# Kernel optimization log

Measured on AMD Instinct MI355X. Metric: run time of the kernel, lower is better.

Reference implementation:

```python
import jax, jax.numpy as jnp
import numpy as np

GX = GY = GZ = 128
VOXEL_DIM = 28  # 1 density + 27 SH coefficients (9 per RGB channel)
NUM_RAYS = 8192
NUM_SAMPLES = 128


def sh_basis(theta, phi):
    """Degree-2 SH basis in the coefficient order used by harmonic():
    [Y_0_0, Y_m1_1, Y_0_1, Y_1_1, Y_m2_2, Y_m1_2, Y_0_2, Y_1_2, Y_2_2]."""
    y00 = 0.5 * jnp.sqrt(1.0 / jnp.pi)
    h3 = 0.5 * jnp.sqrt(3.0 / jnp.pi)
    q5 = 0.25 * jnp.sqrt(5.0 / jnp.pi)
    h15 = 0.5 * jnp.sqrt(15.0 / jnp.pi)
    q15 = 0.25 * jnp.sqrt(15.0 / jnp.pi)
    st, ct = jnp.sin(theta), jnp.cos(theta)
    sp, cp = jnp.sin(phi), jnp.cos(phi)
    return jnp.stack([
        y00 * jnp.ones_like(theta),          # Y_0_0
        h3 * st * sp,                        # Y_m1_1
        h3 * ct,                             # Y_0_1
        h3 * st * cp,                        # Y_1_1
        h15 * st * cp * st * sp,             # Y_m2_2
        h15 * st * sp * ct,                  # Y_m1_2
        q5 * (3.0 * ct * ct - 1.0),          # Y_0_2
        h15 * st * cp * ct,                  # Y_1_2
        q15 * ((st * cp) ** 2 - (st * sp) ** 2),  # Y_2_2
    ])


def trilinear(grid, pos):
    """grid: [GX,GY,GZ,D]; pos: [R,S,3] -> [R,S,D] interpolated features."""
    p0 = jnp.floor(pos).astype(jnp.int32)
    fr = pos - p0.astype(pos.dtype)
    x0, y0, z0 = p0[..., 0], p0[..., 1], p0[..., 2]
    xd, yd, zd = fr[..., 0:1], fr[..., 1:2], fr[..., 2:3]
    c000 = grid[x0, y0, z0]
    c001 = grid[x0, y0, z0 + 1]
    c010 = grid[x0, y0 + 1, z0]
    c011 = grid[x0, y0 + 1, z0 + 1]
    c100 = grid[x0 + 1, y0, z0]
    c101 = grid[x0 + 1, y0, z0 + 1]
    c110 = grid[x0 + 1, y0 + 1, z0]
    c111 = grid[x0 + 1, y0 + 1, z0 + 1]
    c00 = c000 * (1 - xd) + c100 * xd
    c01 = c001 * (1 - xd) + c101 * xd
    c10 = c010 * (1 - xd) + c110 * xd
    c11 = c011 * (1 - xd) + c111 * xd
    c0 = c00 * (1 - yd) + c10 * yd
    c1 = c01 * (1 - yd) + c11 * yd
    return c0 * (1 - zd) + c1 * zd


def setup_inputs() -> dict:
    key = jax.random.key(0)
    k1, k2, k3, k4 = jax.random.split(key, 4)
    voxel_grid = jax.random.uniform(k1, (GX, GY, GZ, VOXEL_DIM), dtype=jnp.float32)
    # sample positions inside [0, G-2] so the +1 corner stays in bounds
    sample_positions = jax.random.uniform(
        k2, (NUM_RAYS, NUM_SAMPLES, 3), dtype=jnp.float32) * (GX - 2)
    sample_distances = jax.random.uniform(
        k3, (NUM_RAYS, NUM_SAMPLES), dtype=jnp.float32) * 0.1
    viewing_angle = jax.random.uniform(k4, (2,), dtype=jnp.float32) * np.pi
    return {
        "voxel_grid": voxel_grid,
        "sample_positions": sample_positions,
        "sample_distances": sample_distances,
        "viewing_angle": viewing_angle,
    }


def reference(voxel_grid, sample_positions, sample_distances, viewing_angle):
    R, S = sample_distances.shape
    feats = trilinear(voxel_grid, sample_positions)          # [R,S,28]
    sigma = feats[..., 0]                                     # [R,S]
    sh_coeffs = feats[..., 1:].reshape(R, S, 3, 9)            # [R,S,3,9]
    basis = sh_basis(viewing_angle[0], viewing_angle[1])      # [9]
    rgb = jnp.einsum('rsck,k->rsc', sh_coeffs, basis)         # [R,S,3]
    tau = sigma * sample_distances                            # [R,S]
    att = jnp.exp(-tau)
    # faithful to channel_opacity_z: transmittance is the CUMULATIVE SUM of
    # exp(-sigma_j * d_j) over j = 0..k (inclusive of current sample)
    transmittance = jnp.cumsum(att, axis=1)
    alpha = 1.0 - att
    weights = transmittance * alpha                           # [R,S]
    return jnp.sum(weights[..., None] * rgb, axis=1)          # [R,3]
```

## Files before the change

kernel.cpp:

```cpp
#include <hip/hip_runtime.h>
#include <math.h>

#define GXD 128
#define GYD 128
#define GZD 128
#define VD 28
#define NRAYS 8192
#define NSAMP 128
#define NVOX (GXD * GYD * GZD)

__global__ __launch_bounds__(256) void predot_grid(
    const float* __restrict__ g,
    const float* __restrict__ ang,
    float4* __restrict__ o)
{
    __shared__ float sb[9];
    if (threadIdx.x == 0) {
        float st, ct, sp, cp;
        sincosf(ang[0], &st, &ct);
        sincosf(ang[1], &sp, &cp);
        sb[0] = 0.28209479177387814f;
        sb[1] = 0.4886025119029199f * st * sp;
        sb[2] = 0.4886025119029199f * ct;
        sb[3] = 0.4886025119029199f * st * cp;
        sb[4] = 1.0925484305920792f * st * cp * st * sp;
        sb[5] = 1.0925484305920792f * st * sp * ct;
        sb[6] = 0.31539156525252005f * (3.0f * ct * ct - 1.0f);
        sb[7] = 1.0925484305920792f * st * cp * ct;
        sb[8] = 0.5462742152960396f * ((st * cp) * (st * cp) - (st * sp) * (st * sp));
    }
    __syncthreads();

    const int v = blockIdx.x * 256 + threadIdx.x;
    const float4* __restrict__ p = (const float4*)(g + (size_t)v * VD);
    float f[28];
    #pragma unroll
    for (int i = 0; i < 7; ++i)
        ((float4*)f)[i] = p[i];

    float r = 0.0f, gg = 0.0f, b = 0.0f;
    #pragma unroll
    for (int k = 0; k < 9; ++k) {
        r  += sb[k] * f[1 + k];
        gg += sb[k] * f[10 + k];
        b  += sb[k] * f[19 + k];
    }
    o[v] = make_float4(f[0], r, gg, b);
}

#define LERP4(a, b, t) make_float4( \
    fmaf((t), (b).x - (a).x, (a).x), \
    fmaf((t), (b).y - (a).y, (a).y), \
    fmaf((t), (b).z - (a).z, (a).z), \
    fmaf((t), (b).w - (a).w, (a).w))

__global__ __launch_bounds__(256) void render(
    const float4* __restrict__ vg,
    const float* __restrict__ pos,
    const float* __restrict__ dist,
    float* __restrict__ out)
{
    __shared__ float4 srgb[2][NSAMP];

    const int tid  = threadIdx.x;
    const int rloc = tid >> 7;
    const int s    = tid & 127;
    const int ray  = blockIdx.x * 2 + rloc;
    const int sidx = ray * NSAMP + s;

    const float px = pos[sidx * 3 + 0];
    const float py = pos[sidx * 3 + 1];
    const float pz = pos[sidx * 3 + 2];
    const int ix = (int)floorf(px);
    const int iy = (int)floorf(py);
    const int iz = (int)floorf(pz);
    const float fx = px - (float)ix;
    const float fy = py - (float)iy;
    const float fz = pz - (float)iz;

    const float4* __restrict__ c = vg + (((size_t)ix * GYD + iy) * GZD + iz);
    const float4 c000 = c[0];
    const float4 c001 = c[1];
    const float4 c010 = c[GZD];
    const float4 c011 = c[GZD + 1];
    const float4 c100 = c[(size_t)GYD * GZD];
    const float4 c101 = c[(size_t)GYD * GZD + 1];
    const float4 c110 = c[(size_t)GYD * GZD + GZD];
    const float4 c111 = c[(size_t)GYD * GZD + GZD + 1];

    const float4 a00 = LERP4(c000, c001, fz);
    const float4 a01 = LERP4(c010, c011, fz);
    const float4 a10 = LERP4(c100, c101, fz);
    const float4 a11 = LERP4(c110, c111, fz);
    const float4 a0  = LERP4(a00, a01, fy);
    const float4 a1  = LERP4(a10, a11, fy);
    const float4 a   = LERP4(a0, a1, fx);

    const float d   = dist[sidx];
    const float att = expf(-a.x * d);
    srgb[rloc][s] = make_float4(att, a.y, a.z, a.w);
    __syncthreads();

    if ((tid & 127) < 64) {
        const int lane = tid & 63;
        const float4 a0v = srgb[rloc][lane];
        const float4 a1v = srgb[rloc][lane + 64];
        const float att0 = a0v.x;
        const float att1 = a1v.x;

        float scan_lo = att0;
        #pragma unroll
        for (int off = 1; off < 64; off <<= 1) {
            const float v = __shfl_up(scan_lo, off, 64);
            if (lane >= off) scan_lo += v;
        }
        const float total_lo = __shfl(scan_lo, 63, 64);

        float scan_hi = att1;
        #pragma unroll
        for (int off = 1; off < 64; off <<= 1) {
            const float v = __shfl_up(scan_hi, off, 64);
            if (lane >= off) scan_hi += v;
        }
        const float w_lo = scan_lo * (1.0f - att0);
        const float w_hi = (total_lo + scan_hi) * (1.0f - att1);

        float o0 = w_lo * a0v.y + w_hi * a1v.y;
        float o1 = w_lo * a0v.z + w_hi * a1v.z;
        float o2 = w_lo * a0v.w + w_hi * a1v.w;

        #pragma unroll
        for (int off = 32; off > 0; off >>= 1) {
            o0 += __shfl_xor(o0, off, 64);
            o1 += __shfl_xor(o1, off, 64);
            o2 += __shfl_xor(o2, off, 64);
        }
        if (lane == 0) {
            out[ray * 3 + 0] = o0;
            out[ray * 3 + 1] = o1;
            out[ray * 3 + 2] = o2;
        }
    }
}

__global__ __launch_bounds__(1024) void plenoxel_fused32(
    const float* __restrict__ grid,
    const float* __restrict__ pos,
    const float* __restrict__ dist,
    const float* __restrict__ ang,
    float* __restrict__ out)
{
    __shared__ float4 srgb[NSAMP];
    const int ray  = blockIdx.x;
    const int tid  = threadIdx.x;
    const int s    = tid >> 3;
    const int subl = tid & 7;
    const int dx   = (subl >> 2) & 1;
    const int dy   = (subl >> 1) & 1;
    const int zh   = subl & 1;

    const float theta = ang[0], phi = ang[1];
    float st, ct, sp, cp;
    sincosf(theta, &st, &ct);
    sincosf(phi,   &sp, &cp);
    float basis[9];
    basis[0] = 0.28209479177387814f;
    basis[1] = 0.4886025119029199f * st * sp;
    basis[2] = 0.4886025119029199f * ct;
    basis[3] = 0.4886025119029199f * st * cp;
    basis[4] = 1.0925484305920792f * st * cp * st * sp;
    basis[5] = 1.0925484305920792f * st * sp * ct;
    basis[6] = 0.31539156525252005f * (3.0f * ct * ct - 1.0f);
    basis[7] = 1.0925484305920792f * st * cp * ct;
    basis[8] = 0.5462742152960396f * ((st * cp) * (st * cp) - (st * sp) * (st * sp));

    const int sidx = ray * NSAMP + s;
    const float px = pos[sidx * 3 + 0];
    const float py = pos[sidx * 3 + 1];
    const float pz = pos[sidx * 3 + 2];
    const int ix = (int)floorf(px);
    const int iy = (int)floorf(py);
    const int iz = (int)floorf(pz);
    const float fx = px - (float)ix;
    const float fy = py - (float)iy;
    const float fz = pz - (float)iz;

    const float w = (dx ? fx : 1.0f - fx) *
                    (dy ? fy : 1.0f - fy) *
                    (zh ? fz : 1.0f - fz);

    const int base = (((ix + dx) * GYD + (iy + dy)) * GZD + (iz + zh)) * VD;
    const float4* __restrict__ q = (const float4*)(grid + base);
    float f[28];
    #pragma unroll
    for (int i = 0; i < 7; ++i)
        ((float4*)f)[i] = q[i];

    float psig = w * f[0];
    float pr = 0.0f, pg = 0.0f, pb = 0.0f;
    #pragma unroll
    for (int k = 0; k < 9; ++k) {
        pr += basis[k] * f[1 + k];
        pg += basis[k] * f[10 + k];
        pb += basis[k] * f[19 + k];
    }
    pr *= w; pg *= w; pb *= w;

    #pragma unroll
    for (int off = 1; off < 8; off <<= 1) {
        psig += __shfl_xor(psig, off, 64);
        pr   += __shfl_xor(pr,   off, 64);
        pg   += __shfl_xor(pg,   off, 64);
        pb   += __shfl_xor(pb,   off, 64);
    }
    if (subl == 0) srgb[s] = make_float4(psig, pr, pg, pb);
    __syncthreads();

    if (tid < 64) {
        const int lane = tid;
        const float4 a0 = srgb[lane];
        const float4 a1 = srgb[lane + 64];
        const float d0 = dist[ray * NSAMP + lane];
        const float d1 = dist[ray * NSAMP + lane + 64];
        const float att0 = expf(-a0.x * d0);
        const float att1 = expf(-a1.x * d1);

        float scan_lo = att0;
        #pragma unroll
        for (int off = 1; off < 64; off <<= 1) {
            const float v = __shfl_up(scan_lo, off, 64);
            if (lane >= off) scan_lo += v;
        }
        const float total_lo = __shfl(scan_lo, 63, 64);
        float scan_hi = att1;
        #pragma unroll
        for (int off = 1; off < 64; off <<= 1) {
            const float v = __shfl_up(scan_hi, off, 64);
            if (lane >= off) scan_hi += v;
        }
        const float w_lo = scan_lo * (1.0f - att0);
        const float w_hi = (total_lo + scan_hi) * (1.0f - att1);

        float o0 = w_lo * a0.y + w_hi * a1.y;
        float o1 = w_lo * a0.z + w_hi * a1.z;
        float o2 = w_lo * a0.w + w_hi * a1.w;
        #pragma unroll
        for (int off = 32; off > 0; off >>= 1) {
            o0 += __shfl_xor(o0, off, 64);
            o1 += __shfl_xor(o1, off, 64);
            o2 += __shfl_xor(o2, off, 64);
        }
        if (lane == 0) {
            out[ray * 3 + 0] = o0;
            out[ray * 3 + 1] = o1;
            out[ray * 3 + 2] = o2;
        }
    }
}

extern "C" void kernel_launch(void* const* d_in, const int* in_sizes, int n_in,
                              void* d_out, int out_size, void* d_ws, size_t ws_size,
                              hipStream_t stream) {
    const float* grid = (const float*)d_in[0];
    const float* pos  = (const float*)d_in[1];
    const float* dist = (const float*)d_in[2];
    const float* ang  = (const float*)d_in[3];
    float* out = (float*)d_out;

    const size_t need = (size_t)NVOX * sizeof(float4);
    if (ws_size >= need) {
        float4* vg = (float4*)d_ws;
        predot_grid<<<NVOX / 256, 256, 0, stream>>>(grid, ang, vg);
        render<<<NRAYS / 2, 256, 0, stream>>>(vg, pos, dist, out);
    } else {
        plenoxel_fused32<<<NRAYS, 1024, 0, stream>>>(grid, pos, dist, ang, out);
    }
}
```

Baseline: 399.8 us.

## Store pre-dotted grid as fp16 in 2x2 xy-interleaved layout

The precomputed per-voxel (sigma, r, g, b) grid is now stored as four half values (8 bytes) instead of float4. It also uses a layout that interleaves 2x2 xy columns along z, so all eight trilinear corners fall in nearby cache lines. This halves workspace traffic and improves gather locality in the render kernel. The cost is fp16 precision on density and colour, which may push the result outside the accuracy tolerance.

```diff
diff --git a/kernel.cpp b/kernel.cpp
--- a/kernel.cpp
+++ b/kernel.cpp
@@ -1,4 +1,5 @@
 #include <hip/hip_runtime.h>
+#include <hip/hip_fp16.h>
 #include <math.h>
 
 #define GXD 128
@@ -9,10 +10,10 @@
 #define NSAMP 128
 #define NVOX (GXD * GYD * GZD)
 
-__global__ __launch_bounds__(256) void predot_grid(
+__global__ __launch_bounds__(256) void predot_quad(
     const float* __restrict__ g,
     const float* __restrict__ ang,
-    float4* __restrict__ o)
+    uint2* __restrict__ o)
 {
     __shared__ float sb[9];
     if (threadIdx.x == 0) {
@@ -31,21 +32,39 @@
     }
     __syncthreads();
 
-    const int v = blockIdx.x * 256 + threadIdx.x;
-    const float4* __restrict__ p = (const float4*)(g + (size_t)v * VD);
-    float f[28];
+    const int xhi = blockIdx.x >> 6;
+    const int yhi = blockIdx.x & 63;
+    const int obase = blockIdx.x << 9;
+
     #pragma unroll
-    for (int i = 0; i < 7; ++i)
-        ((float4*)f)[i] = p[i];
-
-    float r = 0.0f, gg = 0.0f, b = 0.0f;
-    #pragma unroll
-    for (int k = 0; k < 9; ++k) {
-        r  += sb[k] * f[1 + k];
-        gg += sb[k] * f[10 + k];
-        b  += sb[k] * f[19 + k];
-    }
-    o[v] = make_float4(f[0], r, gg, b);
+    for (int q = 0; q < 2; ++q) {
+        const int w   = q * 256 + threadIdx.x;
+        const int col = w >> 7;
+        const int z   = w & 127;
+        const int x   = (xhi << 1) + (col >> 1);
+        const int y   = (yhi << 1) + (col & 1);
+        const size_t v = (((size_t)x << 7) | y) << 7 | z;
+
+        const float4* __restrict__ p = (const float4*)(g + v * VD);
+        float f[28];
+        #pragma unroll
+        for (int i = 0; i < 7; ++i)
+            ((float4*)f)[i] = p[i];
+
+        float r = 0.0f, gg = 0.0f, b = 0.0f;
+        #pragma unroll
+        for (int k = 0; k < 9; ++k) {
+            r  += sb[k] * f[1 + k];
+            gg += sb[k] * f[10 + k];
+            b  += sb[k] * f[19 + k];
+        }
+        const __half2 h0 = __floats2half2_rn(f[0], r);
+        const __half2 h1 = __floats2half2_rn(gg, b);
+        uint2 u;
+        u.x = *(const unsigned*)&h0;
+        u.y = *(const unsigned*)&h1;
+        o[obase + (z << 2) + col] = u;
+    }
 }
 
 #define LERP4(a, b, t) make_float4( \
@@ -54,8 +73,19 @@
     fmaf((t), (b).z - (a).z, (a).z), \
     fmaf((t), (b).w - (a).w, (a).w))
 
-__global__ __launch_bounds__(256) void render(
-    const float4* __restrict__ vg,
+__device__ __forceinline__ float4 fetch_q(const uint2* __restrict__ vg,
+                                          int x, int y, int z)
+{
+    const int p   = ((x >> 1) << 6) | (y >> 1);
+    const int col = ((x & 1) << 1) | (y & 1);
+    const uint2 u = vg[(p << 9) | (z << 2) | col];
+    const float2 sr = __half22float2(*(const __half2*)&u.x);
+    const float2 gb = __half22float2(*(const __half2*)&u.y);
+    return make_float4(sr.x, sr.y, gb.x, gb.y);
+}
+
+__global__ __launch_bounds__(256) void render_q(
+    const uint2* __restrict__ vg,
     const float* __restrict__ pos,
     const float* __restrict__ dist,
     float* __restrict__ out)
@@ -78,15 +108,14 @@
     const float fy = py - (float)iy;
     const float fz = pz - (float)iz;
 
-    const float4* __restrict__ c = vg + (((size_t)ix * GYD + iy) * GZD + iz);
-    const float4 c000 = c[0];
-    const float4 c001 = c[1];
-    const float4 c010 = c[GZD];
-    const float4 c011 = c[GZD + 1];
-    const float4 c100 = c[(size_t)GYD * GZD];
-    const float4 c101 = c[(size_t)GYD * GZD + 1];
-    const float4 c110 = c[(size_t)GYD * GZD + GZD];
-    const float4 c111 = c[(size_t)GYD * GZD + GZD + 1];
+    const float4 c000 = fetch_q(vg, ix,     iy,     iz);
+    const float4 c001 = fetch_q(vg, ix,     iy,     iz + 1);
+    const float4 c010 = fetch_q(vg, ix,     iy + 1, iz);
+    const float4 c011 = fetch_q(vg, ix,     iy + 1, iz + 1);
+    const float4 c100 = fetch_q(vg, ix + 1, iy,     iz);
+    const float4 c101 = fetch_q(vg, ix + 1, iy,     iz + 1);
+    const float4 c110 = fetch_q(vg, ix + 1, iy + 1, iz);
+    const float4 c111 = fetch_q(vg, ix + 1, iy + 1, iz + 1);
 
     const float4 a00 = LERP4(c000, c001, fz);
     const float4 a01 = LERP4(c010, c011, fz);
@@ -267,11 +296,11 @@
     const float* ang  = (const float*)d_in[3];
     float* out = (float*)d_out;
 
-    const size_t need = (size_t)NVOX * sizeof(float4);
+    const size_t need = (size_t)NVOX * sizeof(uint2);
     if (ws_size >= need) {
-        float4* vg = (float4*)d_ws;
-        predot_grid<<<NVOX / 256, 256, 0, stream>>>(grid, ang, vg);
-        render<<<NRAYS / 2, 256, 0, stream>>>(vg, pos, dist, out);
+        uint2* vg = (uint2*)d_ws;
+        predot_quad<<<4096, 256, 0, stream>>>(grid, ang, vg);
+        render_q<<<NRAYS / 2, 256, 0, stream>>>(vg, pos, dist, out);
     } else {
         plenoxel_fused32<<<NRAYS, 1024, 0, stream>>>(grid, pos, dist, ang, out);
     }
```

Measured after the change: 379.7 us. 1.05x faster.
